# Kernel tuning notes

Measured on AMD Instinct MI355X. Metric: run time of the kernel, lower is better.

The kernel has to match this reference:

```python
import jax, jax.numpy as jnp
import numpy as np

NINP, NHID, NOUT = 400, 600, 400
HS = NHID + NOUT          # h_size = nhid + nout
NLEVELS, K, AUX_FREQ = 40, 2, 20
DILATION = [1]


def setup_inputs() -> dict:
    key = jax.random.key(0)
    ks = jax.random.split(key, 6)
    B, T = 8, 256
    bound = 0.01  # matches init_weights normal_(0, 0.01)
    return {
        "X": jax.random.normal(ks[0], (B, NINP, T), jnp.float32),
        "hid": jax.random.normal(ks[1], (B, HS, 1), jnp.float32),
        "cell": jax.random.normal(ks[2], (B, HS, 1), jnp.float32),
        "w1": jax.random.normal(ks[3], (4 * HS, NINP, K), jnp.float32) * bound,
        "w2": jax.random.normal(ks[4], (4 * HS, HS, K), jnp.float32) * bound,
        "b2": jax.random.normal(ks[5], (4 * HS,), jnp.float32) * bound,
    }


def _conv1d(x, w, d):
    # x: [B, Cin, T_padded], w: [Cout, Cin, K] -> [B, Cout, T]
    return jax.lax.conv_general_dilated(
        x, w, window_strides=(1,), padding='VALID', rhs_dilation=(d,),
        dimension_numbers=('NCH', 'OIH', 'NCH'))


def _forward(X, hid, cell, w1, w2, b2):
    B, _, T = X.shape
    ht = jnp.zeros((B, HS, T), X.dtype)
    ct = jnp.zeros((B, HS, T), X.dtype)

    # Input-side convolution is weight-tied and X never changes across levels,
    # so (like the torch dict cache) compute it once per distinct dilation.
    conv1 = {}
    for d in set(DILATION):
        pad = (K - 1) * d
        xp = jnp.pad(X, ((0, 0), (0, 0), (pad, 0)))
        conv1[d] = _conv1d(xp, w1, d)

    aux = []
    for i in range(NLEVELS):
        d = DILATION[i % len(DILATION)]
        pad = (K - 1) * d
        # causal left-pad of the hidden stream, filled with the initial hid
        z1 = jnp.concatenate([jnp.broadcast_to(hid, (B, HS, pad)), ht], axis=2)
        out = conv1[d] + _conv1d(z1, w2, d) + b2[None, :, None]  # [B, 4*HS, T]
        # shifted cell state, first d steps filled with the initial cell
        ct_1 = jnp.concatenate(
            [jnp.broadcast_to(cell, (B, HS, d)), ct[:, :, :-d]], axis=2)
        it = jax.nn.sigmoid(out[:, :HS])
        ot = jax.nn.sigmoid(out[:, HS:2 * HS])
        gt = jnp.tanh(out[:, 2 * HS:3 * HS])
        ft = jax.nn.sigmoid(out[:, 3 * HS:])
        ct = ft * ct_1 + it * gt
        ht = ot * jnp.tanh(ct)
        if i % AUX_FREQ == AUX_FREQ - 1:
            aux.append(ht[:, -NOUT:])  # [B, nout, T]

    out_main = jnp.transpose(ht[:, -NOUT:], (0, 2, 1))            # [B, T, nout]
    hc = (ht[:, :, -1:], ct[:, :, -1:])                            # ([B,HS,1], [B,HS,1])
    aux_outs = jnp.transpose(jnp.stack(aux, axis=0), (1, 0, 3, 2))  # [B, n_aux, T, nout]
    return out_main, hc, aux_outs


def reference(X, hid, cell, w1, w2, b2):
    return _forward(X, hid, cell, w1, w2, b2)
```

## Files before the change

### kernel.cpp

```cpp
#include <hip/hip_runtime.h>
#include <hip/hip_bf16.h>
#include <math.h>

typedef __bf16 bf16;
typedef __bf16 bf16x8 __attribute__((ext_vector_type(8)));
typedef __bf16 bf16x4 __attribute__((ext_vector_type(4)));
typedef float f32x4 __attribute__((ext_vector_type(4)));
typedef unsigned int u32;
typedef u32 u32x4 __attribute__((ext_vector_type(4)));

#define NINP 400
#define HS   1000
#define HP   1024
#define B_   8
#define T_   256
#define NT   2048
#define K2   2048
#define K1   1024
#define M_   4096

#define HT_OFF   819200
#define CT_OFF   827200
#define AUX_OFF  835200

typedef __attribute__((address_space(1))) const void gvoid;
typedef __attribute__((address_space(3))) void lvoid;

__device__ __forceinline__ void async_copy16(void* lds, const void* g) {
  __builtin_amdgcn_global_load_lds((gvoid*)g, (lvoid*)lds, 16, 0, 0);
}

__device__ __forceinline__ float sigm(float x) { return 1.0f / (1.0f + expf(-x)); }


__global__ void repack_w1(const float* __restrict__ w1, bf16* __restrict__ W1q) {
  int idx = blockIdx.x * 256 + threadIdx.x;
  if (idx >= M_ * K1) return;
  int pm = idx >> 10, k = idx & 1023;
  int g = (pm >> 4) & 3;
  int h = (pm >> 7) * 32 + ((pm >> 6) & 1) * 16 + (pm & 15);
  float v = 0.0f;
  if (h < HS) {
    int c = g * HS + h;
    if (k < 512) { if (k < NINP) v = w1[(size_t)c * (NINP * 2) + k * 2 + 0]; }
    else { int j = k - 512; if (j < NINP) v = w1[(size_t)c * (NINP * 2) + j * 2 + 1]; }
  }
  W1q[idx] = (bf16)v;
}

__global__ void repack_w2(const float* __restrict__ w2, bf16* __restrict__ W2q) {
  int idx = blockIdx.x * 256 + threadIdx.x;
  if (idx >= M_ * K2) return;
  int pm = idx >> 11, k = idx & 2047;
  int g = (pm >> 4) & 3;
  int h = (pm >> 7) * 32 + ((pm >> 6) & 1) * 16 + (pm & 15);
  float v = 0.0f;
  if (h < HS) {
    int c = g * HS + h;
    if (k < HP) { if (k < HS) v = w2[(size_t)c * (HS * 2) + k * 2 + 0]; }
    else { int j = k - HP; if (j < HS) v = w2[(size_t)c * (HS * 2) + j * 2 + 1]; }
  }
  W2q[idx] = (bf16)v;
}

__global__ void build_xt(const float* __restrict__ X, bf16* __restrict__ XT) {
  int idx = blockIdx.x * 256 + threadIdx.x;
  if (idx >= NT * K1) return;
  int n = idx >> 10, k = idx & 1023;
  int b = n >> 8, t = n & (T_ - 1);
  float v = 0.0f;
  if (k < 512) { if (k < NINP && t > 0) v = X[((size_t)b * NINP + k) * T_ + t - 1]; }
  else { int j = k - 512; if (j < NINP) v = X[((size_t)b * NINP + j) * T_ + t]; }
  XT[idx] = (bf16)v;
}

__global__ void build_hc(const float* __restrict__ hid, const float* __restrict__ cell,
                         bf16* __restrict__ hidp, float* __restrict__ cellp) {
  int idx = blockIdx.x * 256 + threadIdx.x;
  if (idx >= B_ * HP) return;
  int b = idx >> 10, k = idx & (HP - 1);
  hidp[idx]  = (k < HS) ? (bf16)hid[b * HS + k] : (bf16)0.0f;
  cellp[idx] = (k < HS) ? cell[b * HS + k] : 0.0f;
}


template <bool GATED>
__global__ __launch_bounds__(512, 2) void gemm_step(
    const bf16* __restrict__ A,
    const bf16* __restrict__ Bsrc,
    const bf16* __restrict__ hidp,
    const bf16* __restrict__ CbIn,
    bf16* __restrict__ CbOut,
    const float* __restrict__ b2,
    const bf16* __restrict__ ctprev,
    const float* __restrict__ cellp,
    bf16* __restrict__ ctnew,
    bf16* __restrict__ Hnew,
    int K) {
  __shared__ bf16 As[3][256][64];
  __shared__ bf16 Bs[3][128][64];

  const int tid = threadIdx.x;
  const int lane = tid & 63;
  const int w = tid >> 6;
  const int mh = w >> 1;
  const int nh = w & 1;
  const int dr = lane >> 3, c8 = lane & 7;
  const int swo = ((c8 - dr) & 7) * 8;
  const int quad = lane >> 4, col = lane & 15;

  const int L = blockIdx.y * 16 + blockIdx.x;
  const int bm = (L & 7) * 2 + (L >> 7);
  const int n0 = ((L >> 3) & 15) * 128;

  bf16x4 cb0[4], cb1[4], cb2[4], cb3[4];
  if (GATED) {
#pragma unroll
    for (int nt = 0; nt < 4; ++nt) {
      const int n = n0 + nh * 64 + nt * 16 + col;
      const size_t cb = (size_t)n * 4096 + (size_t)(bm * 256 + mh * 64) + quad * 4;
      cb0[nt] = *(const bf16x4*)&CbIn[cb + 0];
      cb1[nt] = *(const bf16x4*)&CbIn[cb + 16];
      cb2[nt] = *(const bf16x4*)&CbIn[cb + 32];
      cb3[nt] = *(const bf16x4*)&CbIn[cb + 48];
    }
  }

  f32x4 acc[4][4];
#pragma unroll
  for (int i = 0; i < 4; ++i)
#pragma unroll
    for (int j = 0; j < 4; ++j) acc[i][j] = (f32x4){0.f, 0.f, 0.f, 0.f};

  auto stage_h0 = [&](int buf, int it2) {
    const int k0 = it2 << 6;
#pragma unroll
    for (int i = 0; i < 3; ++i) {
      const int r = i * 64 + w * 8 + dr;
      async_copy16(&As[buf][i * 64 + w * 8][0],
                   A + (size_t)(bm * 256 + r) * K + k0 + swo);
    }
  };
  auto stage_h1 = [&](int buf, int it2) {
    const int k0 = it2 << 6;
    {
      const int r = 3 * 64 + w * 8 + dr;
      async_copy16(&As[buf][3 * 64 + w * 8][0],
                   A + (size_t)(bm * 256 + r) * K + k0 + swo);
    }
#pragma unroll
    for (int j = 0; j < 2; ++j) {
      const int r = j * 64 + w * 8 + dr;
      const int n = n0 + r;
      const bf16* bp;
      if (GATED) {
        const int kk = (k0 & (HP - 1)) + swo;
        if (k0 < HP) {
          const int t = n & (T_ - 1);
          bp = (t == 0) ? (hidp + (size_t)(n >> 8) * HP + kk)
                        : (Bsrc + (size_t)(n - 1) * HP + kk);
        } else {
          bp = Bsrc + (size_t)n * HP + kk;
        }
      } else {
        bp = Bsrc + (size_t)n * K + k0 + swo;
      }
      async_copy16(&Bs[buf][j * 64 + w * 8][0], bp);
    }
  };

  const int NIT = K >> 6;
  stage_h0(0, 0); stage_h1(0, 0);
  stage_h0(1, 1); stage_h1(1, 1);
  asm volatile("s_waitcnt vmcnt(6)" ::: "memory");
  __builtin_amdgcn_s_barrier();

  int cur = 0;
  for (int it = 0; it < NIT; ++it) {
    const bool pre = (it + 2 < NIT);
    int nx = cur + 2; if (nx >= 3) nx -= 3;

    {
      bf16x8 av[4], bv[4];
#pragma unroll
      for (int mt = 0; mt < 4; ++mt) {
        const int rA = mh * 64 + mt * 16 + col;
        av[mt] = *(const bf16x8*)&As[cur][rA][((quad + rA) & 7) * 8];
      }
#pragma unroll
      for (int nt = 0; nt < 4; ++nt) {
        const int rB = nh * 64 + nt * 16 + col;
        bv[nt] = *(const bf16x8*)&Bs[cur][rB][((quad + rB) & 7) * 8];
      }
      if (pre) stage_h0(nx, it + 2);
      __builtin_amdgcn_s_barrier();
      asm volatile("s_waitcnt lgkmcnt(0)" ::: "memory");
      __builtin_amdgcn_sched_barrier(0);
      __builtin_amdgcn_s_setprio(1);
#pragma unroll
      for (int mt = 0; mt < 4; ++mt)
#pragma unroll
        for (int nt = 0; nt < 4; ++nt)
          acc[mt][nt] = __builtin_amdgcn_mfma_f32_16x16x32_bf16(av[mt], bv[nt], acc[mt][nt], 0, 0, 0);
      __builtin_amdgcn_s_setprio(0);
      __builtin_amdgcn_s_barrier();
    }

    {
      bf16x8 av[4], bv[4];
#pragma unroll
      for (int mt = 0; mt < 4; ++mt) {
        const int rA = mh * 64 + mt * 16 + col;
        av[mt] = *(const bf16x8*)&As[cur][rA][((4 + quad + rA) & 7) * 8];
      }
#pragma unroll
      for (int nt = 0; nt < 4; ++nt) {
        const int rB = nh * 64 + nt * 16 + col;
        bv[nt] = *(const bf16x8*)&Bs[cur][rB][((4 + quad + rB) & 7) * 8];
      }
      if (pre) stage_h1(nx, it + 2);
      if (pre) asm volatile("s_waitcnt vmcnt(6)" ::: "memory");
      else     asm volatile("s_waitcnt vmcnt(0)" ::: "memory");
      __builtin_amdgcn_s_barrier();
      asm volatile("s_waitcnt lgkmcnt(0)" ::: "memory");
      __builtin_amdgcn_sched_barrier(0);
      __builtin_amdgcn_s_setprio(1);
#pragma unroll
      for (int mt = 0; mt < 4; ++mt)
#pragma unroll
        for (int nt = 0; nt < 4; ++nt)
          acc[mt][nt] = __builtin_amdgcn_mfma_f32_16x16x32_bf16(av[mt], bv[nt], acc[mt][nt], 0, 0, 0);
      __builtin_amdgcn_s_setprio(0);
      __builtin_amdgcn_s_barrier();
    }

    cur = (cur == 2) ? 0 : cur + 1;
  }
  __syncthreads();

  if (!GATED) {
    bf16 (*Csh)[256] = (bf16(*)[256])&As[0][0][0];
#pragma unroll
    for (int mt = 0; mt < 4; ++mt) {
#pragma unroll
      for (int nt = 0; nt < 4; ++nt) {
        const int nloc = nh * 64 + nt * 16 + col;
        bf16x4 v;
#pragma unroll
        for (int j = 0; j < 4; ++j) {
          const int h = bm * 64 + mh * 16 + quad * 4 + j;
          const float bias = (h < HS) ? b2[mt * HS + h] : 0.0f;
          v[j] = (bf16)(acc[mt][nt][j] + bias);
        }
        *(bf16x4*)&Csh[nloc][mh * 64 + mt * 16 + quad * 4] = v;
      }
    }
    __syncthreads();
#pragma unroll
    for (int i2 = 0; i2 < 8; ++i2) {
      const int idx = i2 * 512 + tid;
      const int rrow = idx >> 5, off = idx & 31;
      *(u32x4*)&CbOut[(size_t)(n0 + rrow) * 4096 + bm * 256 + off * 8] =
          *(const u32x4*)&Csh[rrow][off * 8];
    }
  } else {
    bf16 (*Hsh)[64] = (bf16(*)[64])&As[0][0][0];
#pragma unroll
    for (int nt = 0; nt < 4; ++nt) {
      const int nloc = nh * 64 + nt * 16 + col;
      const int n = n0 + nloc;
      const int b = n >> 8;
      const int t = n & (T_ - 1);
      bf16x4 hv;
#pragma unroll
      for (int j = 0; j < 4; ++j) {
        const int h = bm * 64 + mh * 16 + quad * 4 + j;
        const float ci = acc[0][nt][j] + (float)cb0[nt][j];
        const float co = acc[1][nt][j] + (float)cb1[nt][j];
        const float cg = acc[2][nt][j] + (float)cb2[nt][j];
        const float cf = acc[3][nt][j] + (float)cb3[nt][j];
        const float ctold = (t == 0) ? cellp[b * HP + h]
                                     : (float)ctprev[(size_t)h * NT + (n - 1)];
        const float cn = sigm(cf) * ctold + sigm(ci) * tanhf(cg);
        ctnew[(size_t)h * NT + n] = (bf16)cn;
        hv[j] = (bf16)(sigm(co) * tanhf(cn));
      }
      *(bf16x4*)&Hsh[nloc][mh * 16 + quad * 4] = hv;
    }
    __syncthreads();
#pragma unroll
    for (int i2 = 0; i2 < 2; ++i2) {
      const int idx = i2 * 512 + tid;
      const int rrow = idx >> 3, off = idx & 7;
      *(u32x4*)&Hnew[(size_t)(n0 + rrow) * HP + bm * 64 + off * 8] =
          *(const u32x4*)&Hsh[rrow][off * 8];
    }
  }
}


__global__ void aux_kernel(const bf16* __restrict__ H, float* __restrict__ out, int s) {
  int idx = blockIdx.x * 256 + threadIdx.x;
  if (idx >= NT * 100) return;
  int n = idx / 100;
  int o = (idx % 100) * 4;
  int b = n >> 8, t = n & (T_ - 1);
  bf16x4 v = *(const bf16x4*)&H[(size_t)n * HP + 600 + o];
  f32x4 f = {(float)v[0], (float)v[1], (float)v[2], (float)v[3]};
  *(f32x4*)&out[AUX_OFF + ((size_t)((b * 2 + s) * T_ + t)) * 400 + o] = f;
}

__global__ void final_kernel(const bf16* __restrict__ H, const bf16* __restrict__ ct,
                             float* __restrict__ out) {
  int idx = blockIdx.x * 256 + threadIdx.x;
  if (idx < NT * 100) {
    int n = idx / 100;
    int o = (idx % 100) * 4;
    int b = n >> 8, t = n & (T_ - 1);
    bf16x4 v = *(const bf16x4*)&H[(size_t)n * HP + 600 + o];
    f32x4 f = {(float)v[0], (float)v[1], (float)v[2], (float)v[3]};
    *(f32x4*)&out[(size_t)n * 400 + o] = f;
    *(f32x4*)&out[AUX_OFF + ((size_t)((b * 2 + 1) * T_ + t)) * 400 + o] = f;
  } else {
    int j = idx - NT * 100;
    if (j < 8000) {
      int b = j / 1000, h = j % 1000;
      out[HT_OFF + j] = (float)H[(size_t)(b * T_ + 255) * HP + h];
    } else if (j < 16000) {
      int jj = j - 8000;
      int b = jj / 1000, h = jj % 1000;
      out[CT_OFF + jj] = (float)ct[(size_t)h * NT + b * T_ + 255];
    }
  }
}


extern "C" void kernel_launch(void* const* d_in, const int* in_sizes, int n_in,
                              void* d_out, int out_size, void* d_ws, size_t ws_size,
                              hipStream_t stream) {
  const float* X    = (const float*)d_in[0];
  const float* hid  = (const float*)d_in[1];
  const float* cell = (const float*)d_in[2];
  const float* w1   = (const float*)d_in[3];
  const float* w2   = (const float*)d_in[4];
  const float* b2   = (const float*)d_in[5];
  float* out = (float*)d_out;

  char* ws = (char*)d_ws;
  size_t off = 0;
  auto alloc = [&](size_t bytes) {
    void* p = ws + off;
    off += (bytes + 255) & ~(size_t)255;
    return p;
  };
  bf16* W2q    = (bf16*)alloc((size_t)M_ * K2 * 2);
  bf16* CbP    = (bf16*)alloc((size_t)NT * M_ * 2);
  bf16* Hb0    = (bf16*)alloc((size_t)NT * HP * 2);
  bf16* ctb0   = (bf16*)alloc((size_t)HP * NT * 2);
  bf16* hidp   = (bf16*)alloc((size_t)B_ * HP * 2);
  float* cellp = (float*)alloc((size_t)B_ * HP * 4);
  char* R = (char*)alloc((size_t)12 * 1024 * 1024);
  bf16* W1q  = (bf16*)R;
  bf16* XT   = (bf16*)(R + (size_t)8 * 1024 * 1024);
  bf16* ctb1 = (bf16*)R;
  bf16* Hb1  = (bf16*)(R + (size_t)4 * 1024 * 1024);

  bf16* Hb[2]  = {Hb0, Hb1};
  bf16* ctb[2] = {ctb0, ctb1};

  hipMemsetAsync(Hb[0], 0, (size_t)NT * HP * 2, stream);
  hipMemsetAsync(ctb[0], 0, (size_t)HP * NT * 2, stream);

  repack_w1<<<(M_ * K1) / 256, 256, 0, stream>>>(w1, W1q);
  repack_w2<<<(M_ * K2) / 256, 256, 0, stream>>>(w2, W2q);
  build_xt<<<(NT * K1) / 256, 256, 0, stream>>>(X, XT);
  build_hc<<<(B_ * HP) / 256, 256, 0, stream>>>(hid, cell, hidp, cellp);

  dim3 grid(16, 16);
  gemm_step<false><<<grid, 512, 0, stream>>>(W1q, XT, nullptr, nullptr, CbP, b2,
                                             nullptr, nullptr, nullptr, nullptr, K1);
  for (int i = 0; i < 40; ++i) {
    int p = i & 1;
    gemm_step<true><<<grid, 512, 0, stream>>>(W2q, Hb[p], hidp, CbP, nullptr, nullptr,
                                              ctb[p], cellp, ctb[p ^ 1], Hb[p ^ 1], K2);
    if (i == 19) aux_kernel<<<800, 256, 0, stream>>>(Hb[p ^ 1], out, 0);
  }
  final_kernel<<<(NT * 100 + 16000 + 255) / 256, 256, 0, stream>>>(Hb[0], ctb[0], out);
}
```

Baseline: 1.970 ms.

## Shrink GEMM tiles to 128x128 with 256 threads and double-buffered pipeline

Reduces the per-block tile from 256x128 to 128x128 with 4 waves instead of 8, doubling the grid to 512 blocks. The three-stage LDS ring becomes a two-stage double buffer, and global pointers are precomputed before the K loop. The aim is more blocks for better CU occupancy on the 256-CU part, at the cost of lower per-block data reuse and less prefetch depth.

```diff
diff --git a/kernel.cpp b/kernel.cpp
--- a/kernel.cpp
+++ b/kernel.cpp
@@ -85,7 +85,7 @@
 
 
 template <bool GATED>
-__global__ __launch_bounds__(512, 2) void gemm_step(
+__global__ __launch_bounds__(256, 2) void gemm_step(
     const bf16* __restrict__ A,
     const bf16* __restrict__ Bsrc,
     const bf16* __restrict__ hidp,
@@ -97,20 +97,19 @@
     bf16* __restrict__ ctnew,
     bf16* __restrict__ Hnew,
     int K) {
-  __shared__ bf16 As[3][256][64];
-  __shared__ bf16 Bs[3][128][64];
+  __shared__ bf16 As[2][128][64];
+  __shared__ bf16 Bs[2][128][64];
 
   const int tid = threadIdx.x;
   const int lane = tid & 63;
   const int w = tid >> 6;
-  const int mh = w >> 1;
-  const int nh = w & 1;
+  const int mh = w >> 1, nh = w & 1;
   const int dr = lane >> 3, c8 = lane & 7;
   const int swo = ((c8 - dr) & 7) * 8;
   const int quad = lane >> 4, col = lane & 15;
 
-  const int L = blockIdx.y * 16 + blockIdx.x;
-  const int bm = (L & 7) * 2 + (L >> 7);
+  const int L = blockIdx.y * gridDim.x + blockIdx.x;
+  const int bm = (L & 7) * 4 + (L >> 7);
   const int n0 = ((L >> 3) & 15) * 128;
 
   bf16x4 cb0[4], cb1[4], cb2[4], cb3[4];
@@ -118,7 +117,7 @@
 #pragma unroll
     for (int nt = 0; nt < 4; ++nt) {
       const int n = n0 + nh * 64 + nt * 16 + col;
-      const size_t cb = (size_t)n * 4096 + (size_t)(bm * 256 + mh * 64) + quad * 4;
+      const size_t cb = (size_t)n * 4096 + (size_t)(bm * 128 + mh * 64) + quad * 4;
       cb0[nt] = *(const bf16x4*)&CbIn[cb + 0];
       cb1[nt] = *(const bf16x4*)&CbIn[cb + 16];
       cb2[nt] = *(const bf16x4*)&CbIn[cb + 32];
@@ -126,73 +125,57 @@
     }
   }
 
+  const bf16* pa[4];
+  const bf16* pb_lo[4];
+  const bf16* pb_hi[4];
+#pragma unroll
+  for (int j = 0; j < 4; ++j) {
+    const int r = j * 32 + w * 8 + dr;
+    pa[j] = A + (size_t)(bm * 128 + r) * K + swo;
+    const int n = n0 + r;
+    if (GATED) {
+      const int t = n & (T_ - 1);
+      pb_lo[j] = (t == 0) ? (hidp + (size_t)(n >> 8) * HP + swo)
+                          : (Bsrc + (size_t)(n - 1) * HP + swo);
+      pb_hi[j] = Bsrc + (size_t)n * HP + swo - HP;
+    } else {
+      pb_lo[j] = Bsrc + (size_t)n * K + swo;
+      pb_hi[j] = pb_lo[j];
+    }
+  }
+
   f32x4 acc[4][4];
 #pragma unroll
   for (int i = 0; i < 4; ++i)
 #pragma unroll
     for (int j = 0; j < 4; ++j) acc[i][j] = (f32x4){0.f, 0.f, 0.f, 0.f};
 
-  auto stage_h0 = [&](int buf, int it2) {
-    const int k0 = it2 << 6;
-#pragma unroll
-    for (int i = 0; i < 3; ++i) {
-      const int r = i * 64 + w * 8 + dr;
-      async_copy16(&As[buf][i * 64 + w * 8][0],
-                   A + (size_t)(bm * 256 + r) * K + k0 + swo);
+  auto stage = [&](int buf, int it2) {
+#pragma unroll
+    for (int j = 0; j < 4; ++j)
+      async_copy16(&As[buf][j * 32 + w * 8][0], pa[j] + it2 * 64);
+#pragma unroll
+    for (int j = 0; j < 4; ++j) {
+      const bf16* src = (GATED && it2 >= 16) ? pb_hi[j] : pb_lo[j];
+      async_copy16(&Bs[buf][j * 32 + w * 8][0], src + it2 * 64);
     }
   };
-  auto stage_h1 = [&](int buf, int it2) {
-    const int k0 = it2 << 6;
-    {
-      const int r = 3 * 64 + w * 8 + dr;
-      async_copy16(&As[buf][3 * 64 + w * 8][0],
-                   A + (size_t)(bm * 256 + r) * K + k0 + swo);
-    }
-#pragma unroll
-    for (int j = 0; j < 2; ++j) {
-      const int r = j * 64 + w * 8 + dr;
-      const int n = n0 + r;
-      const bf16* bp;
-      if (GATED) {
-        const int kk = (k0 & (HP - 1)) + swo;
-        if (k0 < HP) {
-          const int t = n & (T_ - 1);
-          bp = (t == 0) ? (hidp + (size_t)(n >> 8) * HP + kk)
-                        : (Bsrc + (size_t)(n - 1) * HP + kk);
-        } else {
-          bp = Bsrc + (size_t)n * HP + kk;
-        }
-      } else {
-        bp = Bsrc + (size_t)n * K + k0 + swo;
-      }
-      async_copy16(&Bs[buf][j * 64 + w * 8][0], bp);
-    }
-  };
 
   const int NIT = K >> 6;
-  stage_h0(0, 0); stage_h1(0, 0);
-  stage_h0(1, 1); stage_h1(1, 1);
-  asm volatile("s_waitcnt vmcnt(6)" ::: "memory");
-  __builtin_amdgcn_s_barrier();
-
-  int cur = 0;
-  for (int it = 0; it < NIT; ++it) {
-    const bool pre = (it + 2 < NIT);
-    int nx = cur + 2; if (nx >= 3) nx -= 3;
-
+
+  auto kstep = [&](int it2, int buf) {
     {
       bf16x8 av[4], bv[4];
 #pragma unroll
       for (int mt = 0; mt < 4; ++mt) {
         const int rA = mh * 64 + mt * 16 + col;
-        av[mt] = *(const bf16x8*)&As[cur][rA][((quad + rA) & 7) * 8];
+        av[mt] = *(const bf16x8*)&As[buf][rA][((quad + rA) & 7) * 8];
       }
 #pragma unroll
       for (int nt = 0; nt < 4; ++nt) {
         const int rB = nh * 64 + nt * 16 + col;
-        bv[nt] = *(const bf16x8*)&Bs[cur][rB][((quad + rB) & 7) * 8];
-      }
-      if (pre) stage_h0(nx, it + 2);
+        bv[nt] = *(const bf16x8*)&Bs[buf][rB][((quad + rB) & 7) * 8];
+      }
       __builtin_amdgcn_s_barrier();
       asm volatile("s_waitcnt lgkmcnt(0)" ::: "memory");
       __builtin_amdgcn_sched_barrier(0);
@@ -205,24 +188,27 @@
       __builtin_amdgcn_s_setprio(0);
       __builtin_amdgcn_s_barrier();
     }
-
     {
       bf16x8 av[4], bv[4];
 #pragma unroll
       for (int mt = 0; mt < 4; ++mt) {
         const int rA = mh * 64 + mt * 16 + col;
-        av[mt] = *(const bf16x8*)&As[cur][rA][((4 + quad + rA) & 7) * 8];
+        av[mt] = *(const bf16x8*)&As[buf][rA][((4 + quad + rA) & 7) * 8];
       }
 #pragma unroll
       for (int nt = 0; nt < 4; ++nt) {
         const int rB = nh * 64 + nt * 16 + col;
-        bv[nt] = *(const bf16x8*)&Bs[cur][rB][((4 + quad + rB) & 7) * 8];
-      }
-      if (pre) stage_h1(nx, it + 2);
-      if (pre) asm volatile("s_waitcnt vmcnt(6)" ::: "memory");
-      else     asm volatile("s_waitcnt vmcnt(0)" ::: "memory");
+        bv[nt] = *(const bf16x8*)&Bs[buf][rB][((4 + quad + rB) & 7) * 8];
+      }
+      asm volatile("s_waitcnt lgkmcnt(0)" ::: "memory");
+      __builtin_amdgcn_sched_barrier(0);
       __builtin_amdgcn_s_barrier();
-      asm volatile("s_waitcnt lgkmcnt(0)" ::: "memory");
+      if (it2 + 2 < NIT) {
+        stage(buf, it2 + 2);
+        asm volatile("s_waitcnt vmcnt(8)" ::: "memory");
+      } else {
+        asm volatile("s_waitcnt vmcnt(0)" ::: "memory");
+      }
       __builtin_amdgcn_sched_barrier(0);
       __builtin_amdgcn_s_setprio(1);
 #pragma unroll
@@ -233,13 +219,21 @@
       __builtin_amdgcn_s_setprio(0);
       __builtin_amdgcn_s_barrier();
     }
-
-    cur = (cur == 2) ? 0 : cur + 1;
+  };
+
+  stage(0, 0);
+  stage(1, 1);
+  asm volatile("s_waitcnt vmcnt(8)" ::: "memory");
+  __builtin_amdgcn_s_barrier();
+
+  for (int it2 = 0; it2 < NIT; it2 += 2) {
+    kstep(it2, 0);
+    kstep(it2 + 1, 1);
   }
   __syncthreads();
 
   if (!GATED) {
-    bf16 (*Csh)[256] = (bf16(*)[256])&As[0][0][0];
+    bf16 (*Csh)[128] = (bf16(*)[128])&As[0][0][0];
 #pragma unroll
     for (int mt = 0; mt < 4; ++mt) {
 #pragma unroll
@@ -248,7 +242,7 @@
         bf16x4 v;
 #pragma unroll
         for (int j = 0; j < 4; ++j) {
-          const int h = bm * 64 + mh * 16 + quad * 4 + j;
+          const int h = bm * 32 + mh * 16 + quad * 4 + j;
           const float bias = (h < HS) ? b2[mt * HS + h] : 0.0f;
           v[j] = (bf16)(acc[mt][nt][j] + bias);
         }
@@ -258,13 +252,13 @@
     __syncthreads();
 #pragma unroll
     for (int i2 = 0; i2 < 8; ++i2) {
-      const int idx = i2 * 512 + tid;
-      const int rrow = idx >> 5, off = idx & 31;
-      *(u32x4*)&CbOut[(size_t)(n0 + rrow) * 4096 + bm * 256 + off * 8] =
+      const int idx = i2 * 256 + tid;
+      const int rrow = idx >> 4, off = idx & 15;
+      *(u32x4*)&CbOut[(size_t)(n0 + rrow) * 4096 + bm * 128 + off * 8] =
           *(const u32x4*)&Csh[rrow][off * 8];
     }
   } else {
-    bf16 (*Hsh)[64] = (bf16(*)[64])&As[0][0][0];
+    bf16 (*Hsh)[32] = (bf16(*)[32])&As[0][0][0];
 #pragma unroll
     for (int nt = 0; nt < 4; ++nt) {
       const int nloc = nh * 64 + nt * 16 + col;
@@ -274,7 +268,7 @@
       bf16x4 hv;
 #pragma unroll
       for (int j = 0; j < 4; ++j) {
-        const int h = bm * 64 + mh * 16 + quad * 4 + j;
+        const int h = bm * 32 + mh * 16 + quad * 4 + j;
         const float ci = acc[0][nt][j] + (float)cb0[nt][j];
         const float co = acc[1][nt][j] + (float)cb1[nt][j];
         const float cg = acc[2][nt][j] + (float)cb2[nt][j];
@@ -290,9 +284,9 @@
     __syncthreads();
 #pragma unroll
     for (int i2 = 0; i2 < 2; ++i2) {
-      const int idx = i2 * 512 + tid;
-      const int rrow = idx >> 3, off = idx & 7;
-      *(u32x4*)&Hnew[(size_t)(n0 + rrow) * HP + bm * 64 + off * 8] =
+      const int idx = i2 * 256 + tid;
+      const int rrow = idx >> 2, off = idx & 3;
+      *(u32x4*)&Hnew[(size_t)(n0 + rrow) * HP + bm * 32 + off * 8] =
           *(const u32x4*)&Hsh[rrow][off * 8];
     }
   }
@@ -376,12 +370,12 @@
   build_xt<<<(NT * K1) / 256, 256, 0, stream>>>(X, XT);
   build_hc<<<(B_ * HP) / 256, 256, 0, stream>>>(hid, cell, hidp, cellp);
 
-  dim3 grid(16, 16);
-  gemm_step<false><<<grid, 512, 0, stream>>>(W1q, XT, nullptr, nullptr, CbP, b2,
+  dim3 grid(NT / 128, M_ / 128);
+  gemm_step<false><<<grid, 256, 0, stream>>>(W1q, XT, nullptr, nullptr, CbP, b2,
                                              nullptr, nullptr, nullptr, nullptr, K1);
   for (int i = 0; i < 40; ++i) {
     int p = i & 1;
-    gemm_step<true><<<grid, 512, 0, stream>>>(W2q, Hb[p], hidp, CbP, nullptr, nullptr,
+    gemm_step<true><<<grid, 256, 0, stream>>>(W2q, Hb[p], hidp, CbP, nullptr, nullptr,
                                               ctb[p], cellp, ctb[p ^ 1], Hb[p ^ 1], K2);
     if (i == 19) aux_kernel<<<800, 256, 0, stream>>>(Hb[p ^ 1], out, 0);
   }
```

New measurement: 1.965 ms. About the same (-0.3%).
